# Optimization experiments

Measured on AMD Instinct MI355X. Metric: run time of the kernel, lower is better.

## Reference

```python
import jax, jax.numpy as jnp
import numpy as np

B, S, N, E = 2048, 5, 80, 592
FX, FF, FE, D = 8, 4, 8, 8
H = 800  # GRU hidden


def setup_inputs() -> dict:
    key = jax.random.key(0)
    ks = jax.random.split(key, 20)
    inp = {
        "x": jax.random.normal(ks[0], (B, S, N, FX), jnp.float32),
        "edge_index": jax.random.randint(ks[1], (B, S, 2, E), 0, N, jnp.int32),
        "edge_f": jax.random.normal(ks[2], (B, S, E, FF), jnp.float32),
        "edge_attr": jax.random.normal(ks[3], (B, S, E, FE), jnp.float32),
        # GNN (net_ResEG) params
        "Wx": jax.random.normal(ks[4], (FX, D), jnp.float32) * 0.1,
        "We": jax.random.normal(ks[5], (FE, D), jnp.float32) * 0.1,
        "Wf": jax.random.normal(ks[6], (FF, D), jnp.float32) * 0.1,
        "Wedge": jax.random.normal(ks[7], (2 * D + FE, D), jnp.float32) * 0.1,
        # GRU params (PyTorch layout: [3H, in])
        "w_ih": jax.random.normal(ks[8], (3 * H, N * D + E * D), jnp.float32) * 0.02,
        "w_hh": jax.random.normal(ks[9], (3 * H, H), jnp.float32) * 0.02,
        "b_ih": jnp.zeros((3 * H,), jnp.float32),
        "b_hh": jnp.zeros((3 * H,), jnp.float32),
        # MLP params
        "mlp_w1": jax.random.normal(ks[10], (S * H, 1280), jnp.float32) * 0.02,
        "mlp_b1": jnp.zeros((1280,), jnp.float32),
        "mlp_w2": jax.random.normal(ks[11], (1280, S * 80), jnp.float32) * 0.02,
        "mlp_b2": jnp.zeros((S * 80,), jnp.float32),
    }
    return inp


def _gnn(xg, eig, efg, eag, Wx, We, Wf, Wedge):
    # one graph: xg [N,FX], eig [2,E], efg [E,FF], eag [E,FE]
    src, dst = eig[0], eig[1]
    m = jax.nn.relu(eag @ We + efg @ Wf)            # [E,D] edge messages
    agg = jnp.zeros((N, D), m.dtype).at[dst].add(m)  # scatter-add to nodes
    x_out = xg + jax.nn.relu(xg @ Wx + agg)          # residual node update [N,D]
    feat = jnp.concatenate([x_out[src], x_out[dst], eag], axis=-1)  # [E,2D+FE]
    e_out = eag + jax.nn.relu(feat @ Wedge)          # residual edge update [E,D]
    return x_out, e_out


def _forward(x, edge_index, edge_f, edge_attr, Wx, We, Wf, Wedge,
             w_ih, w_hh, b_ih, b_hh, mlp_w1, mlp_b1, mlp_w2, mlp_b2):
    # normalize edge indices (edge_index[i,j] - edge_index[i,j,0].min())
    mins = edge_index[:, :, 0, :].min(axis=-1)[:, :, None, None]  # [B,S,1,1]
    ei = edge_index - mins

    flat = lambda a: a.reshape((B * S,) + a.shape[2:])
    x1, e1 = jax.vmap(lambda a, b, c, d: _gnn(a, b, c, d, Wx, We, Wf, Wedge))(
        flat(x), flat(ei), flat(edge_f), flat(edge_attr))
    x1 = x1.reshape(B, S, N * D)
    e1 = e1.reshape(B, S, E * D)
    seq = jnp.concatenate([x1, e1], axis=2)  # [B,S,5376]

    # single-layer GRU, batch_first (dropout inactive for 1 layer)
    def step(h, xt):
        gi = xt @ w_ih.T + b_ih   # [B,3H]
        gh = h @ w_hh.T + b_hh
        ir, iz, inn = jnp.split(gi, 3, axis=-1)
        hr, hz, hn = jnp.split(gh, 3, axis=-1)
        r = jax.nn.sigmoid(ir + hr)
        z = jax.nn.sigmoid(iz + hz)
        n = jnp.tanh(inn + r * hn)
        h_new = (1.0 - z) * n + z * h
        return h_new, h_new

    h0 = jnp.zeros((B, H), seq.dtype)
    _, ys = jax.lax.scan(step, h0, jnp.swapaxes(seq, 0, 1))  # [S,B,H]
    y = jnp.swapaxes(ys, 0, 1).reshape(B, S * H)             # [B,4000]

    y = y @ mlp_w1 + mlp_b1
    y = y @ mlp_w2 + mlp_b2
    return y.reshape(B, 80, 5)


def reference(x, edge_index, edge_f, edge_attr, Wx, We, Wf, Wedge,
              w_ih, w_hh, b_ih, b_hh, mlp_w1, mlp_b1, mlp_w2, mlp_b2):
    return _forward(x, edge_index, edge_f, edge_attr, Wx, We, Wf, Wedge,
                    w_ih, w_hh, b_ih, b_hh, mlp_w1, mlp_b1, mlp_w2, mlp_b2)
```

## Files before the change

kernel.cpp:

```cpp
#include <hip/hip_runtime.h>
#include <math.h>

constexpr int B_  = 2048;
constexpr int S_  = 5;
constexpr int N_  = 80;
constexpr int E_  = 592;
constexpr int FX_ = 8;
constexpr int FF_ = 4;
constexpr int FE_ = 8;
constexpr int D_  = 8;
constexpr int H_  = 800;

constexpr int BS_  = B_ * S_;
constexpr int XD_  = N_ * D_;
constexpr int ED_  = E_ * D_;
constexpr int SEQ_ = XD_ + ED_;
constexpr int G3_  = 3 * H_;
constexpr int MIN_ = S_ * H_;
constexpr int MH_  = 1280;
constexpr int MO_  = S_ * 80;

typedef __bf16 bf16_t;
typedef __bf16 bf16x8 __attribute__((ext_vector_type(8)));
typedef float  f32x4  __attribute__((ext_vector_type(4)));

__device__ __forceinline__ float sigmoidf_(float x) {
    return 1.0f / (1.0f + expf(-x));
}

__device__ __forceinline__ void async16(const void* g, void* l) {
    __builtin_amdgcn_global_load_lds(
        (const __attribute__((address_space(1))) unsigned int*)g,
        (__attribute__((address_space(3))) unsigned int*)l,
        16, 0, 0);
}

__global__ __launch_bounds__(256) void gnn_kernel(
    const float* __restrict__ x,
    const int*   __restrict__ ei,
    const float* __restrict__ ef,
    const float* __restrict__ ea,
    const float* __restrict__ Wx,
    const float* __restrict__ We,
    const float* __restrict__ Wf,
    const float* __restrict__ Wedge,
    bf16_t* __restrict__ seq)
{
    const int g   = blockIdx.x;
    const int tid = threadIdx.x;

    __shared__ float sWx[FX_ * D_];
    __shared__ float sWe[FE_ * D_];
    __shared__ float sWf[FF_ * D_];
    __shared__ float sWedge[24 * D_];
    __shared__ float agg[N_ * D_];
    __shared__ float xout[N_ * D_];
    __shared__ int   s_src[E_];
    __shared__ int   s_dst[E_];
    __shared__ int   s_min;

    if (tid == 0) s_min = 0x7fffffff;
    if (tid < FX_ * D_) sWx[tid] = Wx[tid];
    if (tid < FE_ * D_) sWe[tid] = We[tid];
    if (tid < FF_ * D_) sWf[tid] = Wf[tid];
    if (tid < 24 * D_)  sWedge[tid] = Wedge[tid];
    for (int i = tid; i < N_ * D_; i += 256) agg[i] = 0.0f;
    __syncthreads();

    const int* srcp = ei + (size_t)g * 2 * E_;
    const int* dstp = srcp + E_;
    int lmin = 0x7fffffff;
    for (int e = tid; e < E_; e += 256) {
        int sv = srcp[e];
        int dv = dstp[e];
        s_src[e] = sv;
        s_dst[e] = dv;
        lmin = min(lmin, sv);
    }
    atomicMin(&s_min, lmin);
    __syncthreads();
    const int mn = s_min;

    const float* eag = ea + (size_t)g * E_ * FE_;
    const float* efg = ef + (size_t)g * E_ * FF_;
    for (int e = tid; e < E_; e += 256) {
        float a[FE_], f[FF_];
        const float4* ap = (const float4*)(eag + (size_t)e * FE_);
        float4 a0 = ap[0], a1 = ap[1];
        a[0]=a0.x; a[1]=a0.y; a[2]=a0.z; a[3]=a0.w;
        a[4]=a1.x; a[5]=a1.y; a[6]=a1.z; a[7]=a1.w;
        float4 f0 = *(const float4*)(efg + (size_t)e * FF_);
        f[0]=f0.x; f[1]=f0.y; f[2]=f0.z; f[3]=f0.w;

        int dadj = s_dst[e] - mn;
        if (dadj < 0) dadj += N_;

        #pragma unroll
        for (int d = 0; d < D_; d++) {
            float m = 0.0f;
            #pragma unroll
            for (int k = 0; k < FE_; k++) m += a[k] * sWe[k * D_ + d];
            #pragma unroll
            for (int k = 0; k < FF_; k++) m += f[k] * sWf[k * D_ + d];
            m = fmaxf(m, 0.0f);
            atomicAdd(&agg[dadj * D_ + d], m);
        }
    }
    __syncthreads();

    const float* xg = x + (size_t)g * N_ * FX_;
    bf16_t* seqrow = seq + (size_t)g * SEQ_;
    for (int n = tid; n < N_; n += 256) {
        float xi[FX_];
        const float4* xp = (const float4*)(xg + (size_t)n * FX_);
        float4 x0 = xp[0], x1 = xp[1];
        xi[0]=x0.x; xi[1]=x0.y; xi[2]=x0.z; xi[3]=x0.w;
        xi[4]=x1.x; xi[5]=x1.y; xi[6]=x1.z; xi[7]=x1.w;
        #pragma unroll
        for (int d = 0; d < D_; d++) {
            float v = agg[n * D_ + d];
            #pragma unroll
            for (int k = 0; k < FX_; k++) v += xi[k] * sWx[k * D_ + d];
            v = fmaxf(v, 0.0f);
            float o = xi[d] + v;
            xout[n * D_ + d] = o;
            seqrow[n * D_ + d] = (bf16_t)o;
        }
    }
    __syncthreads();

    for (int e = tid; e < E_; e += 256) {
        int sadj = s_src[e] - mn;
        int dadj = s_dst[e] - mn;
        if (dadj < 0) dadj += N_;
        float a[FE_];
        const float4* ap = (const float4*)(eag + (size_t)e * FE_);
        float4 a0 = ap[0], a1 = ap[1];
        a[0]=a0.x; a[1]=a0.y; a[2]=a0.z; a[3]=a0.w;
        a[4]=a1.x; a[5]=a1.y; a[6]=a1.z; a[7]=a1.w;
        const float* xs = &xout[sadj * D_];
        const float* xd = &xout[dadj * D_];
        #pragma unroll
        for (int d = 0; d < D_; d++) {
            float v = 0.0f;
            #pragma unroll
            for (int k = 0; k < D_; k++)  v += xs[k] * sWedge[k * D_ + d];
            #pragma unroll
            for (int k = 0; k < D_; k++)  v += xd[k] * sWedge[(D_ + k) * D_ + d];
            #pragma unroll
            for (int k = 0; k < FE_; k++) v += a[k] * sWedge[(2 * D_ + k) * D_ + d];
            v = fmaxf(v, 0.0f);
            seqrow[XD_ + e * D_ + d] = (bf16_t)(a[d] + v);
        }
    }
}

template <typename OutT>
__global__ __launch_bounds__(256) void mfma_gemm_bt(
    const bf16_t* __restrict__ A,
    const bf16_t* __restrict__ Bm,
    const float*  __restrict__ bias,
    OutT* __restrict__ C,
    int M, int Nn, int K)
{
    __shared__ bf16_t As[128 * 32];
    __shared__ bf16_t Bs[128 * 32];

    const int tid  = threadIdx.x;
    const int wave = tid >> 6;
    const int lane = tid & 63;
    const int m0 = blockIdx.y * 128;
    const int n0 = blockIdx.x * 128;
    const int wm = (wave & 1) * 64;
    const int wn = (wave >> 1) * 64;

    const int srow  = tid >> 2;
    const int skoff = (tid & 3) * 8;

    const int fm = lane & 15;
    const int fk = (lane >> 4) * 8;

    f32x4 acc[4][4] = {};

    const bf16_t* a_ptr0 = A + (size_t)(m0 + srow) * K + skoff;
    const bf16_t* a_ptr1 = a_ptr0 + (size_t)64 * K;
    int brow0 = n0 + srow;      if (brow0 > Nn - 1) brow0 = Nn - 1;
    int brow1 = n0 + 64 + srow; if (brow1 > Nn - 1) brow1 = Nn - 1;
    const bf16_t* b_ptr0 = Bm + (size_t)brow0 * K + skoff;
    const bf16_t* b_ptr1 = Bm + (size_t)brow1 * K + skoff;

    bf16_t* lA0 = &As[srow * 32 + skoff];
    bf16_t* lA1 = &As[(64 + srow) * 32 + skoff];
    bf16_t* lB0 = &Bs[srow * 32 + skoff];
    bf16_t* lB1 = &Bs[(64 + srow) * 32 + skoff];

    for (int k0 = 0; k0 < K; k0 += 32) {
        async16(a_ptr0 + k0, lA0);
        async16(a_ptr1 + k0, lA1);
        async16(b_ptr0 + k0, lB0);
        async16(b_ptr1 + k0, lB1);
        __syncthreads();

        bf16x8 af[4], bfm[4];
        #pragma unroll
        for (int i = 0; i < 4; i++)
            af[i] = *(const bf16x8*)&As[(wm + i * 16 + fm) * 32 + fk];
        #pragma unroll
        for (int j = 0; j < 4; j++)
            bfm[j] = *(const bf16x8*)&Bs[(wn + j * 16 + fm) * 32 + fk];

        #pragma unroll
        for (int i = 0; i < 4; i++)
            #pragma unroll
            for (int j = 0; j < 4; j++)
                acc[i][j] = __builtin_amdgcn_mfma_f32_16x16x32_bf16(
                    af[i], bfm[j], acc[i][j], 0, 0, 0);

        __syncthreads();
    }

    const int crow = (lane >> 4) * 4;
    const int ccol = lane & 15;
    #pragma unroll
    for (int i = 0; i < 4; i++) {
        #pragma unroll
        for (int j = 0; j < 4; j++) {
            int row = m0 + wm + i * 16 + crow;
            int col = n0 + wn + j * 16 + ccol;
            if (col < Nn) {
                float bv = bias[col];
                #pragma unroll
                for (int r = 0; r < 4; r++) {
                    float v = acc[i][j][r] + bv;
                    C[(size_t)(row + r) * Nn + col] = (OutT)v;
                }
            }
        }
    }
}

__global__ __launch_bounds__(256) void f2bf_kernel(
    const float* __restrict__ in, bf16_t* __restrict__ out, int n)
{
    int i = (blockIdx.x * 256 + threadIdx.x) * 4;
    if (i + 3 < n) {
        float4 v = *(const float4*)&in[i];
        out[i + 0] = (bf16_t)v.x;
        out[i + 1] = (bf16_t)v.y;
        out[i + 2] = (bf16_t)v.z;
        out[i + 3] = (bf16_t)v.w;
    } else {
        for (; i < n; i++) out[i] = (bf16_t)in[i];
    }
}

__global__ __launch_bounds__(256) void tconv_kernel(
    const float* __restrict__ in, bf16_t* __restrict__ out, int K, int N)
{
    __shared__ float tile[32][33];
    int k0 = blockIdx.y * 32, n0 = blockIdx.x * 32;
    int tx = threadIdx.x & 31, ty = threadIdx.x >> 5;
    #pragma unroll
    for (int r = 0; r < 32; r += 8) {
        int k = k0 + ty + r, n = n0 + tx;
        tile[ty + r][tx] = (k < K && n < N) ? in[(size_t)k * N + n] : 0.0f;
    }
    __syncthreads();
    #pragma unroll
    for (int r = 0; r < 32; r += 8) {
        int n = n0 + ty + r, k = k0 + tx;
        if (n < N && k < K) out[(size_t)n * K + k] = (bf16_t)tile[tx][ty + r];
    }
}

__global__ __launch_bounds__(256) void gru_gates_kernel(
    const float* __restrict__ gi,
    const float* __restrict__ gh,
    float*  __restrict__ h,
    bf16_t* __restrict__ hb,
    bf16_t* __restrict__ yb,
    int t)
{
    int i = blockIdx.x * blockDim.x + threadIdx.x;
    if (i >= B_ * H_) return;
    int b = i / H_;
    int j = i - b * H_;
    const float* girow = gi + ((size_t)b * S_ + t) * G3_;
    const float* ghrow = gh + (size_t)b * G3_;
    float r = sigmoidf_(girow[j] + ghrow[j]);
    float z = sigmoidf_(girow[H_ + j] + ghrow[H_ + j]);
    float n = tanhf(girow[2 * H_ + j] + r * ghrow[2 * H_ + j]);
    float hp = h[i];
    float hn = (1.0f - z) * n + z * hp;
    h[i] = hn;
    hb[i] = (bf16_t)hn;
    yb[(size_t)b * MIN_ + t * H_ + j] = (bf16_t)hn;
}

extern "C" void kernel_launch(void* const* d_in, const int* in_sizes, int n_in,
                              void* d_out, int out_size, void* d_ws, size_t ws_size,
                              hipStream_t stream) {
    const float* x     = (const float*)d_in[0];
    const int*   ei    = (const int*)  d_in[1];
    const float* ef    = (const float*)d_in[2];
    const float* ea    = (const float*)d_in[3];
    const float* Wx    = (const float*)d_in[4];
    const float* We    = (const float*)d_in[5];
    const float* Wf    = (const float*)d_in[6];
    const float* Wedge = (const float*)d_in[7];
    const float* w_ih  = (const float*)d_in[8];
    const float* w_hh  = (const float*)d_in[9];
    const float* b_ih  = (const float*)d_in[10];
    const float* b_hh  = (const float*)d_in[11];
    const float* w1    = (const float*)d_in[12];
    const float* b1    = (const float*)d_in[13];
    const float* w2    = (const float*)d_in[14];
    const float* b2    = (const float*)d_in[15];
    float* out = (float*)d_out;

    char* p = (char*)d_ws;
    auto alloc = [&](size_t bytes) {
        void* r = (void*)p;
        p += (bytes + 255) & ~(size_t)255;
        return r;
    };
    bf16_t* seq   = (bf16_t*)alloc((size_t)BS_ * SEQ_ * 2);
    bf16_t* wihb  = (bf16_t*)alloc((size_t)G3_ * SEQ_ * 2);
    bf16_t* whhb  = (bf16_t*)alloc((size_t)G3_ * H_ * 2);
    bf16_t* w1t   = (bf16_t*)alloc((size_t)MH_ * MIN_ * 2);
    bf16_t* w2t   = (bf16_t*)alloc((size_t)MO_ * MH_ * 2);
    float*  gi    = (float*) alloc((size_t)BS_ * G3_ * 4);
    float*  gh    = (float*) alloc((size_t)B_ * G3_ * 4);
    float*  h     = (float*) alloc((size_t)B_ * H_ * 4);
    bf16_t* hb    = (bf16_t*)alloc((size_t)B_ * H_ * 2);
    bf16_t* yb    = (bf16_t*)alloc((size_t)B_ * MIN_ * 2);
    bf16_t* t1b   = (bf16_t*)alloc((size_t)B_ * MH_ * 2);

    hipMemsetAsync(h,  0, (size_t)B_ * H_ * sizeof(float), stream);
    hipMemsetAsync(hb, 0, (size_t)B_ * H_ * sizeof(bf16_t), stream);

    {
        int n = G3_ * SEQ_;
        f2bf_kernel<<<(n / 4 + 255) / 256, 256, 0, stream>>>(w_ih, wihb, n);
    }
    {
        int n = G3_ * H_;
        f2bf_kernel<<<(n / 4 + 255) / 256, 256, 0, stream>>>(w_hh, whhb, n);
    }
    {
        dim3 grid((MH_ + 31) / 32, (MIN_ + 31) / 32);
        tconv_kernel<<<grid, 256, 0, stream>>>(w1, w1t, MIN_, MH_);
    }
    {
        dim3 grid((MO_ + 31) / 32, (MH_ + 31) / 32);
        tconv_kernel<<<grid, 256, 0, stream>>>(w2, w2t, MH_, MO_);
    }

    gnn_kernel<<<BS_, 256, 0, stream>>>(x, ei, ef, ea, Wx, We, Wf, Wedge, seq);

    {
        dim3 grid((G3_ + 127) / 128, BS_ / 128);
        mfma_gemm_bt<float><<<grid, 256, 0, stream>>>(seq, wihb, b_ih, gi, BS_, G3_, SEQ_);
    }

    for (int t = 0; t < S_; t++) {
        dim3 grid((G3_ + 127) / 128, B_ / 128);
        mfma_gemm_bt<float><<<grid, 256, 0, stream>>>(hb, whhb, b_hh, gh, B_, G3_, H_);
        gru_gates_kernel<<<(B_ * H_ + 255) / 256, 256, 0, stream>>>(gi, gh, h, hb, yb, t);
    }

    {
        dim3 grid((MH_ + 127) / 128, B_ / 128);
        mfma_gemm_bt<bf16_t><<<grid, 256, 0, stream>>>(yb, w1t, b1, t1b, B_, MH_, MIN_);
    }
    {
        dim3 grid((MO_ + 127) / 128, B_ / 128);
        mfma_gemm_bt<float><<<grid, 256, 0, stream>>>(t1b, w2t, b2, out, B_, MO_, MH_);
    }
}
```

Baseline: 1.548 ms.

## Map one graph per wavefront in GNN kernel and precompute per-node edge projections

The GNN kernel now handles four graphs per block, one per 64-lane wavefront, and replaces the shared atomicMin with a wave shuffle reduction. The edge update is split algebraically: each node's source and destination projections through Wedge are computed once per node and then gathered per edge, instead of being recomputed for every edge. Outputs are written as packed 8-wide bf16 vectors, and the shared arrays are stored feature-major. This is meant to cut redundant FLOPs, per-graph sync overhead and scalar stores, at the cost of fewer threads per graph and source/destination indices being re-read from global memory.

```diff
diff --git a/kernel.cpp b/kernel.cpp
--- a/kernel.cpp
+++ b/kernel.cpp
@@ -35,7 +35,7 @@
         16, 0, 0);
 }
 
-__global__ __launch_bounds__(256) void gnn_kernel(
+__global__ __launch_bounds__(256, 4) void gnn_kernel(
     const float* __restrict__ x,
     const int*   __restrict__ ei,
     const float* __restrict__ ef,
@@ -46,53 +46,50 @@
     const float* __restrict__ Wedge,
     bf16_t* __restrict__ seq)
 {
-    const int g   = blockIdx.x;
-    const int tid = threadIdx.x;
+    const int tid  = threadIdx.x;
+    const int w    = tid >> 6;
+    const int lane = tid & 63;
+    const int g    = blockIdx.x * 4 + w;
 
     __shared__ float sWx[FX_ * D_];
     __shared__ float sWe[FE_ * D_];
     __shared__ float sWf[FF_ * D_];
     __shared__ float sWedge[24 * D_];
-    __shared__ float agg[N_ * D_];
-    __shared__ float xout[N_ * D_];
-    __shared__ int   s_src[E_];
-    __shared__ int   s_dst[E_];
-    __shared__ int   s_min;
-
-    if (tid == 0) s_min = 0x7fffffff;
-    if (tid < FX_ * D_) sWx[tid] = Wx[tid];
-    if (tid < FE_ * D_) sWe[tid] = We[tid];
-    if (tid < FF_ * D_) sWf[tid] = Wf[tid];
-    if (tid < 24 * D_)  sWedge[tid] = Wedge[tid];
-    for (int i = tid; i < N_ * D_; i += 256) agg[i] = 0.0f;
-    __syncthreads();
+    __shared__ float agg[4][D_ * N_];
+    __shared__ float su [4][D_ * N_];
+    __shared__ float sv [4][D_ * N_];
+
+    if (tid < 64) { sWx[tid] = Wx[tid]; sWe[tid] = We[tid]; }
+    if (tid < 32) sWf[tid] = Wf[tid];
+    if (tid < 192) sWedge[tid] = Wedge[tid];
+
+    float* aggw = agg[w];
+    float* uw   = su[w];
+    float* vw   = sv[w];
+    for (int i = lane; i < D_ * N_; i += 64) aggw[i] = 0.0f;
 
     const int* srcp = ei + (size_t)g * 2 * E_;
     const int* dstp = srcp + E_;
+
     int lmin = 0x7fffffff;
-    for (int e = tid; e < E_; e += 256) {
-        int sv = srcp[e];
-        int dv = dstp[e];
-        s_src[e] = sv;
-        s_dst[e] = dv;
-        lmin = min(lmin, sv);
-    }
-    atomicMin(&s_min, lmin);
+    for (int e = lane; e < E_; e += 64) lmin = min(lmin, srcp[e]);
+    #pragma unroll
+    for (int off = 32; off; off >>= 1)
+        lmin = min(lmin, __shfl_xor(lmin, off, 64));
+    const int mn = lmin;
+
     __syncthreads();
-    const int mn = s_min;
 
     const float* eag = ea + (size_t)g * E_ * FE_;
     const float* efg = ef + (size_t)g * E_ * FF_;
-    for (int e = tid; e < E_; e += 256) {
-        float a[FE_], f[FF_];
+    for (int e = lane; e < E_; e += 64) {
         const float4* ap = (const float4*)(eag + (size_t)e * FE_);
         float4 a0 = ap[0], a1 = ap[1];
-        a[0]=a0.x; a[1]=a0.y; a[2]=a0.z; a[3]=a0.w;
-        a[4]=a1.x; a[5]=a1.y; a[6]=a1.z; a[7]=a1.w;
         float4 f0 = *(const float4*)(efg + (size_t)e * FF_);
-        f[0]=f0.x; f[1]=f0.y; f[2]=f0.z; f[3]=f0.w;
-
-        int dadj = s_dst[e] - mn;
+        float a[FE_] = {a0.x, a0.y, a0.z, a0.w, a1.x, a1.y, a1.z, a1.w};
+        float fv[FF_] = {f0.x, f0.y, f0.z, f0.w};
+
+        int dadj = dstp[e] - mn;
         if (dadj < 0) dadj += N_;
 
         #pragma unroll
@@ -101,57 +98,63 @@
             #pragma unroll
             for (int k = 0; k < FE_; k++) m += a[k] * sWe[k * D_ + d];
             #pragma unroll
-            for (int k = 0; k < FF_; k++) m += f[k] * sWf[k * D_ + d];
-            m = fmaxf(m, 0.0f);
-            atomicAdd(&agg[dadj * D_ + d], m);
+            for (int k = 0; k < FF_; k++) m += fv[k] * sWf[k * D_ + d];
+            atomicAdd(&aggw[d * N_ + dadj], fmaxf(m, 0.0f));
         }
     }
     __syncthreads();
 
     const float* xg = x + (size_t)g * N_ * FX_;
     bf16_t* seqrow = seq + (size_t)g * SEQ_;
-    for (int n = tid; n < N_; n += 256) {
-        float xi[FX_];
+    for (int n = lane; n < N_; n += 64) {
         const float4* xp = (const float4*)(xg + (size_t)n * FX_);
         float4 x0 = xp[0], x1 = xp[1];
-        xi[0]=x0.x; xi[1]=x0.y; xi[2]=x0.z; xi[3]=x0.w;
-        xi[4]=x1.x; xi[5]=x1.y; xi[6]=x1.z; xi[7]=x1.w;
+        float xi[FX_] = {x0.x, x0.y, x0.z, x0.w, x1.x, x1.y, x1.z, x1.w};
+
+        float xo[D_];
+        bf16x8 pk;
         #pragma unroll
         for (int d = 0; d < D_; d++) {
-            float v = agg[n * D_ + d];
+            float v = aggw[d * N_ + n];
             #pragma unroll
             for (int k = 0; k < FX_; k++) v += xi[k] * sWx[k * D_ + d];
-            v = fmaxf(v, 0.0f);
-            float o = xi[d] + v;
-            xout[n * D_ + d] = o;
-            seqrow[n * D_ + d] = (bf16_t)o;
+            xo[d] = xi[d] + fmaxf(v, 0.0f);
+            pk[d] = (bf16_t)xo[d];
+        }
+        *(bf16x8*)(seqrow + (size_t)n * D_) = pk;
+
+        #pragma unroll
+        for (int d = 0; d < D_; d++) {
+            float uu = 0.0f, vv = 0.0f;
+            #pragma unroll
+            for (int k = 0; k < D_; k++) {
+                uu += xo[k] * sWedge[k * D_ + d];
+                vv += xo[k] * sWedge[(D_ + k) * D_ + d];
+            }
+            uw[d * N_ + n] = uu;
+            vw[d * N_ + n] = vv;
         }
     }
     __syncthreads();
 
-    for (int e = tid; e < E_; e += 256) {
-        int sadj = s_src[e] - mn;
-        int dadj = s_dst[e] - mn;
-        if (dadj < 0) dadj += N_;
-        float a[FE_];
+    for (int e = lane; e < E_; e += 64) {
         const float4* ap = (const float4*)(eag + (size_t)e * FE_);
         float4 a0 = ap[0], a1 = ap[1];
-        a[0]=a0.x; a[1]=a0.y; a[2]=a0.z; a[3]=a0.w;
-        a[4]=a1.x; a[5]=a1.y; a[6]=a1.z; a[7]=a1.w;
-        const float* xs = &xout[sadj * D_];
-        const float* xd = &xout[dadj * D_];
+        float a[FE_] = {a0.x, a0.y, a0.z, a0.w, a1.x, a1.y, a1.z, a1.w};
+
+        int sadj = srcp[e] - mn;
+        int dadj = dstp[e] - mn;
+        if (dadj < 0) dadj += N_;
+
+        bf16x8 pk;
         #pragma unroll
         for (int d = 0; d < D_; d++) {
-            float v = 0.0f;
-            #pragma unroll
-            for (int k = 0; k < D_; k++)  v += xs[k] * sWedge[k * D_ + d];
-            #pragma unroll
-            for (int k = 0; k < D_; k++)  v += xd[k] * sWedge[(D_ + k) * D_ + d];
-            #pragma unroll
-            for (int k = 0; k < FE_; k++) v += a[k] * sWedge[(2 * D_ + k) * D_ + d];
-            v = fmaxf(v, 0.0f);
-            seqrow[XD_ + e * D_ + d] = (bf16_t)(a[d] + v);
-        }
+            float t = uw[d * N_ + sadj] + vw[d * N_ + dadj];
+            #pragma unroll
+            for (int k = 0; k < FE_; k++) t += a[k] * sWedge[(2 * D_ + k) * D_ + d];
+            pk[d] = (bf16_t)(a[d] + fmaxf(t, 0.0f));
+        }
+        *(bf16x8*)(seqrow + XD_ + (size_t)e * D_) = pk;
     }
 }
 
@@ -356,7 +359,7 @@
         tconv_kernel<<<grid, 256, 0, stream>>>(w2, w2t, MH_, MO_);
     }
 
-    gnn_kernel<<<BS_, 256, 0, stream>>>(x, ei, ef, ea, Wx, We, Wf, Wedge, seq);
+    gnn_kernel<<<BS_ / 4, 256, 0, stream>>>(x, ei, ef, ea, Wx, We, Wf, Wedge, seq);
 
     {
         dim3 grid((G3_ + 127) / 128, BS_ / 128);
```

Measured after the change: 1.505 ms. -2.8%, faster.
